# Kernel tuning notes

Hardware: AMD Instinct MI355X
Metric: run time of the kernel (lower is better)

The kernel has to match this reference:

```python
import jax, jax.numpy as jnp
import numpy as np

MIN_TAU = 1e-3  # max(1e-5, config.CELL_MIN_TAU=0.001)
EPS = 1e-20


def setup_inputs() -> dict:
    key = jax.random.key(0)
    ks = jax.random.split(key, 6)
    B, I, H = 16, 1024, 2048
    return {
        "x_t": jax.random.normal(ks[0], (B, I), jnp.float32),
        "h_prev": jax.random.normal(ks[1], (B, H), jnp.float32),
        "W_ih_w": jax.random.normal(ks[2], (H, I), jnp.float32) * (1.0 / np.sqrt(I)),
        "W_ih_b": jax.random.normal(ks[3], (H,), jnp.float32) * 0.01,
        "W_hh": jax.random.normal(ks[4], (H, H), jnp.float32) * np.sqrt(2.0 / (H + H)),  # xavier-ish
        "temperature": jnp.float32(1.0),
        "hh_mask": jnp.ones((H, H), jnp.float32),
        "u_noise": jax.random.uniform(ks[5], (B, H, H), jnp.float32, minval=EPS, maxval=1.0),
    }


def reference(x_t, h_prev, W_ih_w, W_ih_b, W_hh, temperature, hh_mask, u_noise):
    tau = jnp.maximum(temperature, MIN_TAU)
    input_contrib = x_t @ W_ih_w.T + W_ih_b                 # [B, H]
    logits = (W_hh * hh_mask) / tau                          # [H, H]
    gumbel = -jnp.log(-jnp.log(u_noise))                     # [B, H, H]
    # gumbel_softmax with tau=1.0, hard=False, over last dim
    y = jax.nn.softmax(logits[None, :, :] + gumbel, axis=2)  # [B, H(out), H(in)]
    contrib = jnp.einsum('boh,bh->bo', y, h_prev)            # [B, H]
    return jnp.tanh(input_contrib + contrib)
```

## Files before the change

kernel.cpp:

```cpp
#include <hip/hip_runtime.h>
#include <cstdint>
#include <cstddef>


#define LOG2E 1.4426950408889634f

__global__ __launch_bounds__(256) void precompute_E_kernel(
    const float* __restrict__ Whh, const float* __restrict__ mask,
    const float* __restrict__ temp, float* __restrict__ E, int n4) {
  float tau = fmaxf(temp[0], 1e-3f);
  float sc = LOG2E / tau;
  int stride = gridDim.x * blockDim.x;
  for (int i = blockIdx.x * blockDim.x + threadIdx.x; i < n4; i += stride) {
    float4 w = ((const float4*)Whh)[i];
    float4 m = ((const float4*)mask)[i];
    float4 e;
    e.x = __builtin_amdgcn_exp2f(w.x * m.x * sc);
    e.y = __builtin_amdgcn_exp2f(w.y * m.y * sc);
    e.z = __builtin_amdgcn_exp2f(w.z * m.z * sc);
    e.w = __builtin_amdgcn_exp2f(w.w * m.w * sc);
    ((float4*)E)[i] = e;
  }
}

template <bool PRE>
__global__ __launch_bounds__(256) void rnn_main_kernel(
    const float* __restrict__ x,
    const float* __restrict__ hprev,
    const float* __restrict__ Wih,
    const float* __restrict__ bih,
    const float* __restrict__ Whh,
    const float* __restrict__ temp,
    const float* __restrict__ mask,
    const float* __restrict__ u,
    const float* __restrict__ E,
    float* __restrict__ out)
{
  const int lane = threadIdx.x & 63;
  const int wid  = threadIdx.x >> 6;
  const int row  = (blockIdx.x << 2) + wid;
  const int b = row >> 11;
  const int o = row & 2047;

  const float4* up = (const float4*)(u + ((size_t)row << 11));
  const float4* hp = (const float4*)(hprev + ((size_t)b << 11));

  const float4* ep = nullptr;
  const float4* wp = nullptr;
  const float4* mp = nullptr;
  float sc = 0.f;
  if (PRE) {
    ep = (const float4*)(E + ((size_t)o << 11));
  } else {
    wp = (const float4*)(Whh + ((size_t)o << 11));
    mp = (const float4*)(mask + ((size_t)o << 11));
    float tau = fmaxf(temp[0], 1e-3f);
    sc = LOG2E / tau;
  }

  float s = 0.f, wsum = 0.f;
#pragma unroll
  for (int it = 0; it < 8; ++it) {
    int idx = (it << 6) + lane;
    float4 uu = up[idx];
    float4 hh = hp[idx];
    float4 ee;
    if (PRE) {
      ee = ep[idx];
    } else {
      float4 w = wp[idx];
      float4 m = mp[idx];
      ee.x = __builtin_amdgcn_exp2f(w.x * m.x * sc);
      ee.y = __builtin_amdgcn_exp2f(w.y * m.y * sc);
      ee.z = __builtin_amdgcn_exp2f(w.z * m.z * sc);
      ee.w = __builtin_amdgcn_exp2f(w.w * m.w * sc);
    }
    float w0 = ee.x * __builtin_amdgcn_rcpf(__builtin_amdgcn_logf(uu.x));
    float w1 = ee.y * __builtin_amdgcn_rcpf(__builtin_amdgcn_logf(uu.y));
    float w2 = ee.z * __builtin_amdgcn_rcpf(__builtin_amdgcn_logf(uu.z));
    float w3 = ee.w * __builtin_amdgcn_rcpf(__builtin_amdgcn_logf(uu.w));
    s += w0; wsum = fmaf(w0, hh.x, wsum);
    s += w1; wsum = fmaf(w1, hh.y, wsum);
    s += w2; wsum = fmaf(w2, hh.z, wsum);
    s += w3; wsum = fmaf(w3, hh.w, wsum);
  }

  const float4* xp  = (const float4*)(x + ((size_t)b << 10));
  const float4* wip = (const float4*)(Wih + ((size_t)o << 10));
  float ic = 0.f;
#pragma unroll
  for (int it = 0; it < 4; ++it) {
    int idx = (it << 6) + lane;
    float4 xx = xp[idx];
    float4 ww = wip[idx];
    ic = fmaf(xx.x, ww.x, ic);
    ic = fmaf(xx.y, ww.y, ic);
    ic = fmaf(xx.z, ww.z, ic);
    ic = fmaf(xx.w, ww.w, ic);
  }

#pragma unroll
  for (int off = 32; off > 0; off >>= 1) {
    s    += __shfl_xor(s, off, 64);
    wsum += __shfl_xor(wsum, off, 64);
    ic   += __shfl_xor(ic, off, 64);
  }

  if (lane == 0) {
    float contrib = wsum / s;
    out[row] = tanhf(ic + bih[o] + contrib);
  }
}

extern "C" void kernel_launch(void* const* d_in, const int* in_sizes, int n_in,
                              void* d_out, int out_size, void* d_ws, size_t ws_size,
                              hipStream_t stream) {
  const float* x     = (const float*)d_in[0];
  const float* hprev = (const float*)d_in[1];
  const float* Wih   = (const float*)d_in[2];
  const float* bih   = (const float*)d_in[3];
  const float* Whh   = (const float*)d_in[4];
  const float* temp  = (const float*)d_in[5];
  const float* mask  = (const float*)d_in[6];
  const float* u     = (const float*)d_in[7];
  float* out = (float*)d_out;

  const size_t EBYTES = (size_t)2048 * 2048 * sizeof(float);
  if (ws_size >= EBYTES) {
    float* E = (float*)d_ws;
    precompute_E_kernel<<<2048, 256, 0, stream>>>(Whh, mask, temp, E, 2048 * 2048 / 4);
    rnn_main_kernel<true><<<8192, 256, 0, stream>>>(x, hprev, Wih, bih, Whh, temp, mask, u, E, out);
  } else {
    rnn_main_kernel<false><<<8192, 256, 0, stream>>>(x, hprev, Wih, bih, Whh, temp, mask, u, nullptr, out);
  }
}
```

Measured before the change: 401.9 us.

## Fuse exp precompute into main kernel with per-row shared-memory E across batch

Drops the separate precompute kernel and its 16 MB workspace round trip. Each block now handles one output row o for all 16 batches: it computes exp(W_hh*mask/tau) for that row into shared memory once, then 16 wavefronts reuse it while streaming u_noise. This removes a kernel launch and the write and re-read of E. In exchange it uses 1024-thread blocks with a barrier, and each wave's u reads are now 16 MB apart across the block.

```diff
diff --git a/kernel.cpp b/kernel.cpp
--- a/kernel.cpp
+++ b/kernel.cpp
@@ -5,26 +5,7 @@
 
 #define LOG2E 1.4426950408889634f
 
-__global__ __launch_bounds__(256) void precompute_E_kernel(
-    const float* __restrict__ Whh, const float* __restrict__ mask,
-    const float* __restrict__ temp, float* __restrict__ E, int n4) {
-  float tau = fmaxf(temp[0], 1e-3f);
-  float sc = LOG2E / tau;
-  int stride = gridDim.x * blockDim.x;
-  for (int i = blockIdx.x * blockDim.x + threadIdx.x; i < n4; i += stride) {
-    float4 w = ((const float4*)Whh)[i];
-    float4 m = ((const float4*)mask)[i];
-    float4 e;
-    e.x = __builtin_amdgcn_exp2f(w.x * m.x * sc);
-    e.y = __builtin_amdgcn_exp2f(w.y * m.y * sc);
-    e.z = __builtin_amdgcn_exp2f(w.z * m.z * sc);
-    e.w = __builtin_amdgcn_exp2f(w.w * m.w * sc);
-    ((float4*)E)[i] = e;
-  }
-}
-
-template <bool PRE>
-__global__ __launch_bounds__(256) void rnn_main_kernel(
+__global__ __launch_bounds__(1024) void rnn_fused_kernel(
     const float* __restrict__ x,
     const float* __restrict__ hprev,
     const float* __restrict__ Wih,
@@ -33,30 +14,32 @@
     const float* __restrict__ temp,
     const float* __restrict__ mask,
     const float* __restrict__ u,
-    const float* __restrict__ E,
     float* __restrict__ out)
 {
-  const int lane = threadIdx.x & 63;
-  const int wid  = threadIdx.x >> 6;
-  const int row  = (blockIdx.x << 2) + wid;
-  const int b = row >> 11;
-  const int o = row & 2047;
+  __shared__ float e_row[2048];
 
-  const float4* up = (const float4*)(u + ((size_t)row << 11));
-  const float4* hp = (const float4*)(hprev + ((size_t)b << 11));
+  const int o    = blockIdx.x;
+  const int tid  = threadIdx.x;
+  const int lane = tid & 63;
+  const int b    = tid >> 6;
 
-  const float4* ep = nullptr;
-  const float4* wp = nullptr;
-  const float4* mp = nullptr;
-  float sc = 0.f;
-  if (PRE) {
-    ep = (const float4*)(E + ((size_t)o << 11));
-  } else {
-    wp = (const float4*)(Whh + ((size_t)o << 11));
-    mp = (const float4*)(mask + ((size_t)o << 11));
-    float tau = fmaxf(temp[0], 1e-3f);
-    sc = LOG2E / tau;
+  {
+    const float tau = fmaxf(temp[0], 1e-3f);
+    const float sc  = LOG2E / tau;
+    const float2* wp = (const float2*)(Whh  + ((size_t)o << 11));
+    const float2* mp = (const float2*)(mask + ((size_t)o << 11));
+    float2 ww = wp[tid];
+    float2 mm = mp[tid];
+    float2 ee;
+    ee.x = __builtin_amdgcn_exp2f(ww.x * mm.x * sc);
+    ee.y = __builtin_amdgcn_exp2f(ww.y * mm.y * sc);
+    ((float2*)e_row)[tid] = ee;
   }
+  __syncthreads();
+
+  const float4* up  = (const float4*)(u + ((size_t)((b << 11) + o) << 11));
+  const float4* hp  = (const float4*)(hprev + ((size_t)b << 11));
+  const float4* ep4 = (const float4*)e_row;
 
   float s = 0.f, wsum = 0.f;
 #pragma unroll
@@ -64,17 +47,7 @@
     int idx = (it << 6) + lane;
     float4 uu = up[idx];
     float4 hh = hp[idx];
-    float4 ee;
-    if (PRE) {
-      ee = ep[idx];
-    } else {
-      float4 w = wp[idx];
-      float4 m = mp[idx];
-      ee.x = __builtin_amdgcn_exp2f(w.x * m.x * sc);
-      ee.y = __builtin_amdgcn_exp2f(w.y * m.y * sc);
-      ee.z = __builtin_amdgcn_exp2f(w.z * m.z * sc);
-      ee.w = __builtin_amdgcn_exp2f(w.w * m.w * sc);
-    }
+    float4 ee = ep4[idx];
     float w0 = ee.x * __builtin_amdgcn_rcpf(__builtin_amdgcn_logf(uu.x));
     float w1 = ee.y * __builtin_amdgcn_rcpf(__builtin_amdgcn_logf(uu.y));
     float w2 = ee.z * __builtin_amdgcn_rcpf(__builtin_amdgcn_logf(uu.z));
@@ -85,7 +58,7 @@
     s += w3; wsum = fmaf(w3, hh.w, wsum);
   }
 
-  const float4* xp  = (const float4*)(x + ((size_t)b << 10));
+  const float4* xp  = (const float4*)(x   + ((size_t)b << 10));
   const float4* wip = (const float4*)(Wih + ((size_t)o << 10));
   float ic = 0.f;
 #pragma unroll
@@ -101,14 +74,13 @@
 
 #pragma unroll
   for (int off = 32; off > 0; off >>= 1) {
-    s    += __shfl_xor(s, off, 64);
+    s    += __shfl_xor(s,    off, 64);
     wsum += __shfl_xor(wsum, off, 64);
-    ic   += __shfl_xor(ic, off, 64);
+    ic   += __shfl_xor(ic,   off, 64);
   }
 
   if (lane == 0) {
-    float contrib = wsum / s;
-    out[row] = tanhf(ic + bih[o] + contrib);
+    out[(b << 11) + o] = tanhf(ic + bih[o] + wsum / s);
   }
 }
 
@@ -125,12 +97,6 @@
   const float* u     = (const float*)d_in[7];
   float* out = (float*)d_out;
 
-  const size_t EBYTES = (size_t)2048 * 2048 * sizeof(float);
-  if (ws_size >= EBYTES) {
-    float* E = (float*)d_ws;
-    precompute_E_kernel<<<2048, 256, 0, stream>>>(Whh, mask, temp, E, 2048 * 2048 / 4);
-    rnn_main_kernel<true><<<8192, 256, 0, stream>>>(x, hprev, Wih, bih, Whh, temp, mask, u, E, out);
-  } else {
-    rnn_main_kernel<false><<<8192, 256, 0, stream>>>(x, hprev, Wih, bih, Whh, temp, mask, u, nullptr, out);
-  }
+  rnn_fused_kernel<<<2048, 1024, 0, stream>>>(x, hprev, Wih, bih, Whh, temp,
+                                              mask, u, out);
 }
```

After: 401.4 us. About the same (-0.1%).
